# Kernel tuning notes

Hardware: AMD Instinct MI355X
Metric: run time of the kernel (lower is better)

Reference implementation:

```python
import jax, jax.numpy as jnp
import numpy as np

BIN_SIZE = 256  # init arg bin_size
K = 16          # init arg k


def setup_inputs() -> dict:
    key = jax.random.key(0)
    k1, k2 = jax.random.split(key)
    x = jax.random.normal(k1, (2, 8192, 256), dtype=jnp.float32)          # (B, N, D)
    codebook = jax.random.normal(k2, (256, 32), dtype=jnp.float32)        # (D, max_num_bins//2)
    return {"x": x, "codebook": codebook}


def reference(x, codebook):
    B, N, D = x.shape
    n_bins = N // BIN_SIZE
    # LSH binning: project onto random hyperplanes, argmax over [proj, -proj]
    mul = jnp.matmul(x, codebook[:, : n_bins // 2])          # (B, N, n_bins//2)
    cmul = jnp.concatenate([mul, -mul], axis=-1)             # (B, N, n_bins)
    bin_idx = jnp.argmax(cmul, axis=-1)                      # (B, N)
    # stable sort points by bin id -> equal-size bins (matches torch.argsort)
    bins_split = jnp.argsort(bin_idx, axis=-1).reshape(B, n_bins, BIN_SIZE)
    # gather points into bins
    pts = jnp.take_along_axis(x, bins_split.reshape(B, N, 1), axis=1)
    pts = pts.reshape(B, n_bins, BIN_SIZE, D)
    # per-bin dense similarity + sigmoid
    dm = jax.nn.sigmoid(jnp.einsum('bnid,bnjd->bnik'.replace('k', 'j'), pts, pts))  # (B, n_bins, BIN, BIN)
    vals, inds = jax.lax.top_k(dm, K)                        # (B, n_bins, BIN, K)
    # map local bin indices back to global point indices
    flat_split = bins_split.reshape(B, N)
    bin_off = jnp.arange(n_bins, dtype=inds.dtype)[None, :, None, None] * BIN_SIZE
    gdst = jnp.take_along_axis(flat_split, (bin_off + inds).reshape(B, -1), axis=1)
    gdst = gdst.reshape(B, n_bins, BIN_SIZE, K)
    gsrc = jnp.broadcast_to(bins_split[..., None], vals.shape)
    bidx = jnp.broadcast_to(jnp.arange(B)[:, None, None, None], vals.shape)
    # coalesced sparse adjacency, represented densely (duplicates summed like coalesce())
    out = jnp.zeros((B, N, N), x.dtype).at[bidx, gsrc, gdst].add(vals)
    return out
```

## Files before the change

### kernel.cpp

```cpp
#include <hip/hip_runtime.h>
#include <math.h>

#define BB    2
#define NN    8192
#define DD    256
#define NBINS 32
#define BINSZ 256
#define NPROJ 16
#define TOPK  16
#define NPTS  (BB * NN)

typedef float vf4 __attribute__((ext_vector_type(4)));

__global__ __launch_bounds__(64) void k_bins(const float* __restrict__ x,
                                             const float* __restrict__ cb,
                                             int* __restrict__ bin_idx) {
    __shared__ float cbt[DD][NPROJ];
    const int t = threadIdx.x;
    for (int q = t; q < DD * 4; q += 64) {
        int d = q >> 2, j4 = q & 3;
        float4 v = *(const float4*)(cb + d * 32 + j4 * 4);
        cbt[d][j4 * 4 + 0] = v.x; cbt[d][j4 * 4 + 1] = v.y;
        cbt[d][j4 * 4 + 2] = v.z; cbt[d][j4 * 4 + 3] = v.w;
    }
    __syncthreads();

    const int p = blockIdx.x * 64 + t;
    const float* xr = x + (size_t)p * DD;

    double a[NPROJ];
#pragma unroll
    for (int j = 0; j < NPROJ; ++j) a[j] = 0.0;

    for (int d0 = 0; d0 < DD; d0 += 4) {
        float4 xv = *(const float4*)(xr + d0);
        float xs[4] = {xv.x, xv.y, xv.z, xv.w};
#pragma unroll
        for (int dd = 0; dd < 4; ++dd) {
            double xd = (double)xs[dd];
#pragma unroll
            for (int j = 0; j < NPROJ; ++j)
                a[j] = fma((double)cbt[d0 + dd][j], xd, a[j]);
        }
    }

    float bv = -INFINITY; int bj = 0;
#pragma unroll
    for (int j = 0; j < NPROJ; ++j) {
        float m = (float)a[j];
        if (m > bv) { bv = m; bj = j; }
    }
#pragma unroll
    for (int j = 0; j < NPROJ; ++j) {
        float m = -(float)a[j];
        if (m > bv) { bv = m; bj = j + NPROJ; }
    }
    bin_idx[p] = bj;
}

__global__ __launch_bounds__(256) void k_sort(const int* __restrict__ bin_idx,
                                              int* __restrict__ order) {
    __shared__ int c[NBINS][256];
    __shared__ int base[NBINS];
    const int t = threadIdx.x;
    const int b = blockIdx.x;
    const int* bi = bin_idx + b * NN;

    for (int j = 0; j < NBINS; ++j) c[j][t] = 0;
    __syncthreads();

    const int i0 = t * 32;
    for (int i = 0; i < 32; ++i) c[bi[i0 + i]][t]++;
    __syncthreads();

    if (t < NBINS) {
        int s = 0;
        for (int q = 0; q < 256; ++q) s += c[t][q];
        base[t] = s;
    }
    __syncthreads();
    if (t == 0) {
        int run = 0;
        for (int j = 0; j < NBINS; ++j) { int tmp = base[j]; base[j] = run; run += tmp; }
    }
    __syncthreads();
    if (t < NBINS) {
        int run = base[t];
        for (int q = 0; q < 256; ++q) { int tmp = c[t][q]; c[t][q] = run; run += tmp; }
    }
    __syncthreads();

    int* ob = order + b * NN;
    for (int i = 0; i < 32; ++i) {
        int gi = i0 + i;
        int bb = bi[gi];
        int pos = c[bb][t]++;
        ob[pos] = gi;
    }
}

#define RT 32
__global__ __launch_bounds__(256, 2) void k_sim(const float* __restrict__ x,
                                                const int* __restrict__ order,
                                                float* __restrict__ out) {
    __shared__ int   idx[BINSZ];
    __shared__ float Af[RT][36];
    __shared__ float S[RT][BINSZ + 1];
    __shared__ float tvs[RT][TOPK];
    __shared__ int   tds[RT][TOPK];

    const int t   = threadIdx.x;
    const int bid = blockIdx.x;
    const int b   = bid >> 8;
    const int bin = (bid >> 3) & 31;
    const int r0  = (bid & 7) * RT;

    idx[t] = order[b * NN + bin * BINSZ + t];
    __syncthreads();

    const int rh = t >> 7;
    const int c  = t & 127;
    const float* xb  = x + (size_t)b * NN * DD;
    const float* xc0 = xb + (size_t)idx[c] * DD;
    const float* xc1 = xb + (size_t)idx[c + 128] * DD;

    const int sr = t >> 3;
    const int qg = t & 7;
    const float* arow = xb + (size_t)idx[r0 + sr] * DD + qg * 4;

    double acc[16][2];
#pragma unroll
    for (int r = 0; r < 16; ++r) { acc[r][0] = 0.0; acc[r][1] = 0.0; }

    const vf4 z4 = (vf4)0.0f;

#pragma unroll 1
    for (int it = 0; it < 8; ++it) {
        const int k0 = it * 32;

        float4 av = *(const float4*)(arow + k0);
        float4 b0v[8], b1v[8];
#pragma unroll
        for (int q = 0; q < 8; ++q) b0v[q] = *(const float4*)(xc0 + k0 + q * 4);
#pragma unroll
        for (int q = 0; q < 8; ++q) b1v[q] = *(const float4*)(xc1 + k0 + q * 4);

        {
            const int zr = it * 4;
#pragma unroll
            for (int rr = 0; rr < 4; ++rr) {
                vf4* orow = (vf4*)(out + ((size_t)b * NN + idx[r0 + zr + rr]) * NN);
#pragma unroll
                for (int j = 0; j < 8; ++j)
                    __builtin_nontemporal_store(z4, orow + j * 256 + t);
            }
        }

        *(float4*)&Af[sr][qg * 4] = av;
        __syncthreads();

#pragma unroll
        for (int dd4 = 0; dd4 < 8; ++dd4) {
            const float4 bq0 = b0v[dd4], bq1 = b1v[dd4];
            const double c00 = (double)bq0.x, c01 = (double)bq0.y,
                         c02 = (double)bq0.z, c03 = (double)bq0.w;
            const double c10 = (double)bq1.x, c11 = (double)bq1.y,
                         c12 = (double)bq1.z, c13 = (double)bq1.w;
#pragma unroll
            for (int r = 0; r < 16; ++r) {
                const float4 afv = *(const float4*)&Af[rh * 16 + r][dd4 * 4];
                const double a0 = (double)afv.x, a1 = (double)afv.y,
                             a2 = (double)afv.z, a3 = (double)afv.w;
                double s0 = acc[r][0];
                s0 = fma(a0, c00, s0); s0 = fma(a1, c01, s0);
                s0 = fma(a2, c02, s0); s0 = fma(a3, c03, s0);
                acc[r][0] = s0;
                double s1 = acc[r][1];
                s1 = fma(a0, c10, s1); s1 = fma(a1, c11, s1);
                s1 = fma(a2, c12, s1); s1 = fma(a3, c13, s1);
                acc[r][1] = s1;
            }
        }
        __syncthreads();
    }

#pragma unroll
    for (int r = 0; r < 16; ++r) {
        float s0 = (float)acc[r][0];
        S[rh * 16 + r][c]       = 1.0f / (1.0f + expf(-s0));
        float s1 = (float)acc[r][1];
        S[rh * 16 + r][c + 128] = 1.0f / (1.0f + expf(-s1));
    }
    __syncthreads();

    if (t < RT) {
        float tv[TOPK]; int ti[TOPK];
#pragma unroll
        for (int q = 0; q < TOPK; ++q) { tv[q] = -INFINITY; ti[q] = 0; }
        for (int cc = 0; cc < BINSZ; ++cc) {
            float v = S[t][cc];
            if (v > tv[TOPK - 1]) {
                tv[TOPK - 1] = v; ti[TOPK - 1] = cc;
#pragma unroll
                for (int q = TOPK - 1; q > 0; --q) {
                    if (tv[q] > tv[q - 1]) {
                        float fv = tv[q]; tv[q] = tv[q - 1]; tv[q - 1] = fv;
                        int   fi = ti[q]; ti[q] = ti[q - 1]; ti[q - 1] = fi;
                    }
                }
            }
        }
#pragma unroll
        for (int q = 0; q < TOPK; ++q) {
            tvs[t][q] = tv[q];
            tds[t][q] = idx[ti[q]];
        }
    }
    __syncthreads();

#pragma unroll
    for (int p = t; p < RT * TOPK; p += 256) {
        int r = p >> 4, q = p & 15;
        float* orow = out + ((size_t)b * NN + idx[r0 + r]) * NN;
        orow[tds[r][q]] = tvs[r][q];
    }
}

extern "C" void kernel_launch(void* const* d_in, const int* in_sizes, int n_in,
                              void* d_out, int out_size, void* d_ws, size_t ws_size,
                              hipStream_t stream) {
    const float* x  = (const float*)d_in[0];
    const float* cb = (const float*)d_in[1];
    float* out      = (float*)d_out;

    int* bin_idx = (int*)d_ws;
    int* order   = bin_idx + NPTS;

    k_bins<<<NPTS / 64, 64, 0, stream>>>(x, cb, bin_idx);
    k_sort<<<BB, 256, 0, stream>>>(bin_idx, order);
    k_sim<<<BB * NBINS * 8, 256, 0, stream>>>(x, order, out);
}
```

Before: 680.9 us.

## Stage bin tile in shared memory and use 8x4 register tiles in similarity kernel

The similarity kernel now loads all 256 bin rows for each 32-wide K slice into shared memory once per block and computes an 8x4 outer-product register tile per thread. Before, each thread streamed two column rows from global memory and used a 16x2 tile. This lowers per-thread global loads and raises the FMA-to-load ratio, at the cost of more LDS traffic and an extra barrier per iteration. The binning kernel also stores the codebook as doubles in shared memory, which removes per-FMA float-to-double conversions but doubles the LDS footprint.

```diff
diff --git a/kernel.cpp b/kernel.cpp
--- a/kernel.cpp
+++ b/kernel.cpp
@@ -15,13 +15,15 @@
 __global__ __launch_bounds__(64) void k_bins(const float* __restrict__ x,
                                              const float* __restrict__ cb,
                                              int* __restrict__ bin_idx) {
-    __shared__ float cbt[DD][NPROJ];
+    __shared__ double cbd[DD][NPROJ];
     const int t = threadIdx.x;
     for (int q = t; q < DD * 4; q += 64) {
         int d = q >> 2, j4 = q & 3;
         float4 v = *(const float4*)(cb + d * 32 + j4 * 4);
-        cbt[d][j4 * 4 + 0] = v.x; cbt[d][j4 * 4 + 1] = v.y;
-        cbt[d][j4 * 4 + 2] = v.z; cbt[d][j4 * 4 + 3] = v.w;
+        cbd[d][j4 * 4 + 0] = (double)v.x;
+        cbd[d][j4 * 4 + 1] = (double)v.y;
+        cbd[d][j4 * 4 + 2] = (double)v.z;
+        cbd[d][j4 * 4 + 3] = (double)v.w;
     }
     __syncthreads();
 
@@ -40,7 +42,7 @@
             double xd = (double)xs[dd];
 #pragma unroll
             for (int j = 0; j < NPROJ; ++j)
-                a[j] = fma((double)cbt[d0 + dd][j], xd, a[j]);
+                a[j] = fma(cbd[d0 + dd][j], xd, a[j]);
         }
     }
 
@@ -104,7 +106,7 @@
                                                 const int* __restrict__ order,
                                                 float* __restrict__ out) {
     __shared__ int   idx[BINSZ];
-    __shared__ float Af[RT][36];
+    __shared__ float Bt[BINSZ][36];
     __shared__ float S[RT][BINSZ + 1];
     __shared__ float tvs[RT][TOPK];
     __shared__ int   tds[RT][TOPK];
@@ -118,19 +120,22 @@
     idx[t] = order[b * NN + bin * BINSZ + t];
     __syncthreads();
 
-    const int rh = t >> 7;
-    const int c  = t & 127;
-    const float* xb  = x + (size_t)b * NN * DD;
-    const float* xc0 = xb + (size_t)idx[c] * DD;
-    const float* xc1 = xb + (size_t)idx[c + 128] * DD;
-
-    const int sr = t >> 3;
-    const int qg = t & 7;
-    const float* arow = xb + (size_t)idx[r0 + sr] * DD + qg * 4;
-
-    double acc[16][2];
-#pragma unroll
-    for (int r = 0; r < 16; ++r) { acc[r][0] = 0.0; acc[r][1] = 0.0; }
+    const float* xb = x + (size_t)b * NN * DD;
+
+    const int sr_ = t >> 3, sc = t & 7;
+    const float* srow[8];
+#pragma unroll
+    for (int q = 0; q < 8; ++q)
+        srow[q] = xb + (size_t)idx[sr_ + 32 * q] * DD + sc * 4;
+
+    const int rg    = t >> 6;
+    const int cbase = t & 63;
+
+    double acc[8][4];
+#pragma unroll
+    for (int r = 0; r < 8; ++r)
+#pragma unroll
+        for (int k = 0; k < 4; ++k) acc[r][k] = 0.0;
 
     const vf4 z4 = (vf4)0.0f;
 
@@ -138,12 +143,9 @@
     for (int it = 0; it < 8; ++it) {
         const int k0 = it * 32;
 
-        float4 av = *(const float4*)(arow + k0);
-        float4 b0v[8], b1v[8];
-#pragma unroll
-        for (int q = 0; q < 8; ++q) b0v[q] = *(const float4*)(xc0 + k0 + q * 4);
-#pragma unroll
-        for (int q = 0; q < 8; ++q) b1v[q] = *(const float4*)(xc1 + k0 + q * 4);
+        float4 st[8];
+#pragma unroll
+        for (int q = 0; q < 8; ++q) st[q] = *(const float4*)(srow[q] + k0);
 
         {
             const int zr = it * 4;
@@ -156,41 +158,55 @@
             }
         }
 
-        *(float4*)&Af[sr][qg * 4] = av;
         __syncthreads();
+#pragma unroll
+        for (int q = 0; q < 8; ++q)
+            *(float4*)&Bt[sr_ + 32 * q][sc * 4] = st[q];
+        __syncthreads();
 
 #pragma unroll
         for (int dd4 = 0; dd4 < 8; ++dd4) {
-            const float4 bq0 = b0v[dd4], bq1 = b1v[dd4];
-            const double c00 = (double)bq0.x, c01 = (double)bq0.y,
-                         c02 = (double)bq0.z, c03 = (double)bq0.w;
-            const double c10 = (double)bq1.x, c11 = (double)bq1.y,
-                         c12 = (double)bq1.z, c13 = (double)bq1.w;
-#pragma unroll
-            for (int r = 0; r < 16; ++r) {
-                const float4 afv = *(const float4*)&Af[rh * 16 + r][dd4 * 4];
-                const double a0 = (double)afv.x, a1 = (double)afv.y,
-                             a2 = (double)afv.z, a3 = (double)afv.w;
-                double s0 = acc[r][0];
-                s0 = fma(a0, c00, s0); s0 = fma(a1, c01, s0);
-                s0 = fma(a2, c02, s0); s0 = fma(a3, c03, s0);
-                acc[r][0] = s0;
-                double s1 = acc[r][1];
-                s1 = fma(a0, c10, s1); s1 = fma(a1, c11, s1);
-                s1 = fma(a2, c12, s1); s1 = fma(a3, c13, s1);
-                acc[r][1] = s1;
+            float4 af[8];
+#pragma unroll
+            for (int rr = 0; rr < 8; ++rr)
+                af[rr] = *(const float4*)&Bt[r0 + rg * 8 + rr][dd4 * 4];
+            float4 bf[4];
+#pragma unroll
+            for (int k = 0; k < 4; ++k)
+                bf[k] = *(const float4*)&Bt[cbase + 64 * k][dd4 * 4];
+
+#pragma unroll
+            for (int e = 0; e < 4; ++e) {
+                float ae[8], be[4];
+#pragma unroll
+                for (int rr = 0; rr < 8; ++rr)
+                    ae[rr] = (e == 0) ? af[rr].x : (e == 1) ? af[rr].y
+                           : (e == 2) ? af[rr].z : af[rr].w;
+#pragma unroll
+                for (int k = 0; k < 4; ++k)
+                    be[k] = (e == 0) ? bf[k].x : (e == 1) ? bf[k].y
+                          : (e == 2) ? bf[k].z : bf[k].w;
+                double ad[8], bd[4];
+#pragma unroll
+                for (int rr = 0; rr < 8; ++rr) ad[rr] = (double)ae[rr];
+#pragma unroll
+                for (int k = 0; k < 4; ++k)    bd[k]  = (double)be[k];
+#pragma unroll
+                for (int rr = 0; rr < 8; ++rr)
+#pragma unroll
+                    for (int k = 0; k < 4; ++k)
+                        acc[rr][k] = fma(ad[rr], bd[k], acc[rr][k]);
             }
         }
-        __syncthreads();
-    }
-
-#pragma unroll
-    for (int r = 0; r < 16; ++r) {
-        float s0 = (float)acc[r][0];
-        S[rh * 16 + r][c]       = 1.0f / (1.0f + expf(-s0));
-        float s1 = (float)acc[r][1];
-        S[rh * 16 + r][c + 128] = 1.0f / (1.0f + expf(-s1));
-    }
+    }
+
+#pragma unroll
+    for (int rr = 0; rr < 8; ++rr)
+#pragma unroll
+        for (int k = 0; k < 4; ++k) {
+            float s32 = (float)acc[rr][k];
+            S[rg * 8 + rr][cbase + 64 * k] = 1.0f / (1.0f + expf(-s32));
+        }
     __syncthreads();
 
     if (t < RT) {
```

Result: slower. 696.5 us (+2.3%).
